# Optimization experiments

Hardware: AMD Instinct MI355X
Metric: run time of the kernel (lower is better)

Reference implementation:

```python
import jax, jax.numpy as jnp
import numpy as np

B = 128        # graphs in batch
GW = 30        # grid width (nodes per graph = GW*GW)
IW = 90        # image width = 3*GW for k=7,s=3,p=2 conv transpose
C_IN = 32
HID = [64, 64, 32]
R = 8          # num relations
NB = 4         # num bases
N = B * GW * GW          # 115200 nodes
E = N * 8                # 921600 edges
NEG_SLOPE = 0.01         # F.leaky_relu default


def setup_inputs() -> dict:
    key = jax.random.key(0)
    ks = jax.random.split(key, 24)
    inp = {
        "features": jax.random.normal(ks[0], (N, C_IN), jnp.float32),
        "src": jax.random.randint(ks[1], (E,), 0, N),
        "dst": jax.random.randint(ks[2], (E,), 0, N),
        "etypes": jax.random.randint(ks[3], (E,), 0, R),
        "norm": jax.random.uniform(ks[4], (E,), jnp.float32),
    }
    dims = [C_IN] + HID
    for l in range(3):
        din, dout = dims[l], dims[l + 1]
        s = 1.0 / np.sqrt(din)
        inp[f"bases{l}"] = jax.random.normal(ks[5 + 4 * l], (NB, din, dout), jnp.float32) * s
        inp[f"comp{l}"] = jax.random.normal(ks[6 + 4 * l], (R, NB), jnp.float32) * (1.0 / np.sqrt(NB))
        inp[f"loop{l}"] = jax.random.normal(ks[7 + 4 * l], (din, dout), jnp.float32) * s
        inp[f"bias{l}"] = jnp.zeros((dout,), jnp.float32)
    inp["conv_w"] = jax.random.normal(ks[20], (HID[-1], 1, 7, 7), jnp.float32) * 0.05  # torch ConvT layout (Cin,Cout,kH,kW)
    inp["conv_b"] = jnp.zeros((1,), jnp.float32)
    return inp


def _rel_graph_conv(h, bases, comp, loop_w, bias, src, dst, etypes, norm, act):
    # basis decomposition: W_r = sum_b comp[r,b] * bases[b]   -> (R, in, out)
    W = jnp.einsum("rb,bio->rio", comp, bases)
    # project every node by every relation weight, then gather per edge
    proj = jnp.einsum("ni,rio->nro", h, W)          # (N, R, out)
    msg = proj[src, etypes] * norm[:, None]          # (E, out)
    agg = jax.ops.segment_sum(msg, dst, num_segments=h.shape[0])
    out = agg + h @ loop_w + bias                    # self-loop + bias (DGL defaults)
    return act(out)


def _conv_transpose(x, w_torch, b, stride, pad):
    # torch ConvTranspose2d(w: (Cin,Cout,kH,kW)) == dilated conv with flipped kernel
    k = w_torch.shape[-1]
    w = jnp.flip(w_torch, (2, 3)).transpose(1, 0, 2, 3)  # -> OIHW
    p = k - 1 - pad
    y = jax.lax.conv_general_dilated(
        x, w, window_strides=(1, 1), padding=[(p, p), (p, p)],
        lhs_dilation=(stride, stride),
        dimension_numbers=("NCHW", "OIHW", "NCHW"))
    return y + b[None, :, None, None]


def reference(features, src, dst, etypes, norm,
              bases0, comp0, loop0, bias0,
              bases1, comp1, loop1, bias1,
              bases2, comp2, loop2, bias2,
              conv_w, conv_b):
    leaky = lambda x: jnp.where(x >= 0, x, NEG_SLOPE * x)
    h = _rel_graph_conv(features, bases0, comp0, loop0, bias0, src, dst, etypes, norm, leaky)
    h = _rel_graph_conv(h, bases1, comp1, loop1, bias1, src, dst, etypes, norm, leaky)
    logits = _rel_graph_conv(h, bases2, comp2, loop2, bias2, src, dst, etypes, norm, jax.nn.sigmoid)
    # every graph has exactly GW*GW nodes -> vectorized decode (replaces per-graph loop)
    x = logits.reshape(B, GW, GW, HID[-1]).transpose(0, 3, 1, 2)  # (B, C, GW, GW)
    y = jax.nn.sigmoid(_conv_transpose(x, conv_w, conv_b, stride=3, pad=2))  # (B,1,IW,IW)
    return y.reshape(B, IW, IW)
```

## Files before the change

### kernel.cpp

```cpp
#include <hip/hip_runtime.h>
#include <hip/hip_bf16.h>

#define B_GR   128
#define GWID   30
#define IWID   90
#define C_IN   32
#define R_REL  8
#define NBAS   4
#define N_NODES (B_GR*GWID*GWID)
#define E_EDGES (N_NODES*8)
#define NEG_SLOPE 0.01f

#define SCAN_BLOCKS (N_NODES/256)

typedef __attribute__((ext_vector_type(8))) __bf16 bf16x8;
typedef __attribute__((ext_vector_type(4))) float f32x4;

__global__ void k_bases_t(const float* __restrict__ bases, __bf16* __restrict__ Bt,
                          int din, int dout) {
    int idx = blockIdx.x*256 + threadIdx.x;
    int tot = NBAS*din*dout;
    if (idx >= tot) return;
    int b = idx/(dout*din), rem = idx%(dout*din);
    int c = rem/din, k = rem%din;
    Bt[idx] = (__bf16)bases[((size_t)b*din + k)*dout + c];
}
__global__ void k_loop_t(const float* __restrict__ loopw, __bf16* __restrict__ loopt,
                         int din, int dout) {
    int idx = blockIdx.x*256 + threadIdx.x;
    if (idx >= din*dout) return;
    int c = idx/din, k = idx%din;
    loopt[idx] = (__bf16)loopw[(size_t)k*dout + c];
}
__global__ void k_feat2bf(const float* __restrict__ f, __bf16* __restrict__ fb) {
    int i = blockIdx.x*256 + threadIdx.x;
    if (i >= N_NODES*C_IN/8) return;
    const float4* p = (const float4*)(f + (size_t)i*8);
    float4 a = p[0], b = p[1];
    bf16x8 o;
    o[0]=(__bf16)a.x; o[1]=(__bf16)a.y; o[2]=(__bf16)a.z; o[3]=(__bf16)a.w;
    o[4]=(__bf16)b.x; o[5]=(__bf16)b.y; o[6]=(__bf16)b.z; o[7]=(__bf16)b.w;
    *(bf16x8*)(fb + (size_t)i*8) = o;
}

__global__ void k_deg(const int* __restrict__ dst, int* __restrict__ deg) {
    int e = blockIdx.x*256 + threadIdx.x;
    if (e < E_EDGES) atomicAdd(&deg[dst[e]], 1);
}
__global__ __launch_bounds__(256) void k_scan1(const int* __restrict__ deg,
                                               int* __restrict__ rowptr,
                                               int* __restrict__ bsum) {
    __shared__ int s[256], s2[256];
    const int tid = threadIdx.x, gid = blockIdx.x*256 + tid;
    int v = deg[gid];
    s[tid] = v;
    __syncthreads();
    int* cur = s; int* nxt = s2;
    for (int d = 1; d < 256; d <<= 1) {
        int val = cur[tid];
        if (tid >= d) val += cur[tid - d];
        nxt[tid] = val;
        __syncthreads();
        int* t = cur; cur = nxt; nxt = t;
    }
    rowptr[gid] = cur[tid] - v;
    if (tid == 255) bsum[blockIdx.x] = cur[255];
}
__global__ __launch_bounds__(512) void k_scan2(int* __restrict__ bsum, int* __restrict__ rowptr) {
    __shared__ int s[512], s2[512];
    const int tid = threadIdx.x;
    int v = (tid < SCAN_BLOCKS) ? bsum[tid] : 0;
    s[tid] = v;
    __syncthreads();
    int* cur = s; int* nxt = s2;
    for (int d = 1; d < 512; d <<= 1) {
        int val = cur[tid];
        if (tid >= d) val += cur[tid - d];
        nxt[tid] = val;
        __syncthreads();
        int* t = cur; cur = nxt; nxt = t;
    }
    if (tid < SCAN_BLOCKS) bsum[tid] = cur[tid] - v;
    if (tid == 0) rowptr[N_NODES] = E_EDGES;
}
__global__ void k_scan3(int* __restrict__ rowptr, const int* __restrict__ bsum,
                        int* __restrict__ cursor) {
    int gid = blockIdx.x*256 + threadIdx.x;
    int v = rowptr[gid] + bsum[blockIdx.x];
    rowptr[gid] = v;
    cursor[gid] = v;
}
__global__ void k_scatter_pack(const int* __restrict__ src, const int* __restrict__ dst,
                               const int* __restrict__ et, const float* __restrict__ norm,
                               int* __restrict__ cursor, int2* __restrict__ pmeta) {
    int e = blockIdx.x*256 + threadIdx.x;
    if (e < E_EDGES) {
        int pos = atomicAdd(&cursor[dst[e]], 1);
        int2 m;
        m.x = src[e] | (et[e] << 24);
        m.y = __float_as_int(norm[e]);
        pmeta[pos] = m;
    }
}

template<int DIN, int DOUT, int ACT, int IN_F32, int OUT_F32, int MINW>
__global__ __launch_bounds__(256, MINW) void k_fusedb(
        const void* __restrict__ hin, const __bf16* __restrict__ Bt,
        const __bf16* __restrict__ loopt, const float* __restrict__ bias,
        const float* __restrict__ comp, const int* __restrict__ rowptr,
        const int2* __restrict__ pmeta, void* __restrict__ hout) {
    constexpr int KS = DIN/32;
    constexpr int NF = DOUT/16;
    const int tid = threadIdx.x;
    const int w = tid >> 6, l = tid & 63;
    const int m = l & 15, g = l >> 4;
    const int nb = blockIdx.x*64 + w*16;
    const int node = nb + m;

    f32x4 acc[NF];
    #pragma unroll
    for (int nf = 0; nf < NF; ++nf) acc[nf] = (f32x4){0.f,0.f,0.f,0.f};

    float ka[NBAS][KS][8];
    #pragma unroll
    for (int b = 0; b < NBAS; ++b)
        #pragma unroll
        for (int ks = 0; ks < KS; ++ks)
            #pragma unroll
            for (int c = 0; c < 8; ++c) ka[b][ks][c] = 0.f;

    const int jb = rowptr[node], je = rowptr[node+1];
    int2 mt = pmeta[jb];
    for (int j = jb; j < je; ++j) {
        const int2 mtn = pmeta[j+1];
        const int p = mt.x & 0xFFFFFF;
        const int et = ((unsigned)mt.x) >> 24;
        const float nm = __int_as_float(mt.y);
        const float4 cw = *(const float4*)(comp + et*NBAS);
        const float w0 = nm*cw.x, w1 = nm*cw.y, w2 = nm*cw.z, w3 = nm*cw.w;
        float hv[KS][8];
        if (IN_F32) {
            const float* hp = (const float*)hin + (size_t)p*DIN + g*8;
            #pragma unroll
            for (int ks = 0; ks < KS; ++ks) {
                float4 v0 = *(const float4*)(hp + ks*32);
                float4 v1 = *(const float4*)(hp + ks*32 + 4);
                hv[ks][0]=v0.x; hv[ks][1]=v0.y; hv[ks][2]=v0.z; hv[ks][3]=v0.w;
                hv[ks][4]=v1.x; hv[ks][5]=v1.y; hv[ks][6]=v1.z; hv[ks][7]=v1.w;
            }
        } else {
            const __bf16* hp = (const __bf16*)hin + (size_t)p*DIN + g*8;
            #pragma unroll
            for (int ks = 0; ks < KS; ++ks) {
                bf16x8 v = *(const bf16x8*)(hp + ks*32);
                #pragma unroll
                for (int c = 0; c < 8; ++c) hv[ks][c] = (float)v[c];
            }
        }
        #pragma unroll
        for (int ks = 0; ks < KS; ++ks) {
            #pragma unroll
            for (int c = 0; c < 8; ++c) {
                ka[0][ks][c] += w0*hv[ks][c];
                ka[1][ks][c] += w1*hv[ks][c];
                ka[2][ks][c] += w2*hv[ks][c];
                ka[3][ks][c] += w3*hv[ks][c];
            }
        }
        mt = mtn;
    }

    #pragma unroll
    for (int b = 0; b < NBAS; ++b) {
        #pragma unroll
        for (int ks = 0; ks < KS; ++ks) {
            bf16x8 fa;
            #pragma unroll
            for (int c = 0; c < 8; ++c) fa[c] = (__bf16)ka[b][ks][c];
            #pragma unroll
            for (int nf = 0; nf < NF; ++nf) {
                bf16x8 fb = *(const bf16x8*)(Bt + ((size_t)b*DOUT + nf*16 + m)*DIN
                                             + ks*32 + g*8);
                acc[nf] = __builtin_amdgcn_mfma_f32_16x16x32_bf16(fa, fb, acc[nf], 0, 0, 0);
            }
        }
    }

    #pragma unroll
    for (int ks = 0; ks < KS; ++ks) {
        bf16x8 fa;
        if (IN_F32) {
            const float* hp = (const float*)hin + (size_t)node*DIN + ks*32 + g*8;
            float4 v0 = *(const float4*)hp;
            float4 v1 = *(const float4*)(hp + 4);
            fa[0]=(__bf16)v0.x; fa[1]=(__bf16)v0.y; fa[2]=(__bf16)v0.z; fa[3]=(__bf16)v0.w;
            fa[4]=(__bf16)v1.x; fa[5]=(__bf16)v1.y; fa[6]=(__bf16)v1.z; fa[7]=(__bf16)v1.w;
        } else {
            fa = *(const bf16x8*)((const __bf16*)hin + (size_t)node*DIN + ks*32 + g*8);
        }
        #pragma unroll
        for (int nf = 0; nf < NF; ++nf) {
            bf16x8 fb = *(const bf16x8*)(loopt + (size_t)(nf*16 + m)*DIN + ks*32 + g*8);
            acc[nf] = __builtin_amdgcn_mfma_f32_16x16x32_bf16(fa, fb, acc[nf], 0, 0, 0);
        }
    }

    #pragma unroll
    for (int nf = 0; nf < NF; ++nf) {
        const int col = nf*16 + m;
        const float bv = bias[col];
        #pragma unroll
        for (int ri = 0; ri < 4; ++ri) {
            const int orow = nb + g*4 + ri;
            float v = acc[nf][ri] + bv;
            if (ACT == 0) v = (v >= 0.f) ? v : NEG_SLOPE*v;
            else          v = 1.f/(1.f + __expf(-v));
            if (OUT_F32) ((float*)hout)[(size_t)orow*DOUT + col] = v;
            else         ((__bf16*)hout)[(size_t)orow*DOUT + col] = (__bf16)v;
        }
    }
}

__global__ __launch_bounds__(256) void k_convt_f32(const float* __restrict__ logits,
        const float* __restrict__ w, const float* __restrict__ cb, float* __restrict__ out) {
    __shared__ float s_w[49*32];
    const int tid = threadIdx.x;
    for (int idx = tid; idx < 49*32; idx += 256) {
        int tap = idx/32, c = idx%32;
        s_w[tap*32 + c] = w[c*49 + tap];
    }
    __syncthreads();
    int gidx = blockIdx.x*256 + tid;
    if (gidx >= B_GR*IWID*IWID) return;
    int b = gidx/(IWID*IWID);
    int rem = gidx%(IWID*IWID);
    int oy = rem/IWID, ox = rem%IWID;

    const int py = (oy+2)%3, qy = (oy+2)/3;
    const int px = (ox+2)%3, qx = (ox+2)/3;

    float acc = cb[0];
    #pragma unroll
    for (int sy = 0; sy < 3; ++sy) {
        const int ky = py + 3*sy;
        const int iy = qy - sy;
        if (ky > 6 || iy < 0 || iy >= GWID) continue;
        #pragma unroll
        for (int sx = 0; sx < 3; ++sx) {
            const int kx = px + 3*sx;
            const int ix = qx - sx;
            if (kx > 6 || ix < 0 || ix >= GWID) continue;
            const float4* xp = (const float4*)&logits[(((size_t)b*GWID + iy)*GWID + ix)*32];
            const float4* wp = (const float4*)&s_w[(ky*7 + kx)*32];
            #pragma unroll
            for (int c4 = 0; c4 < 8; ++c4) {
                float4 xv = xp[c4], wv = wp[c4];
                acc += xv.x*wv.x + xv.y*wv.y + xv.z*wv.z + xv.w*wv.w;
            }
        }
    }
    out[gidx] = 1.f/(1.f + __expf(-acc));
}

extern "C" void kernel_launch(void* const* d_in, const int* in_sizes, int n_in,
                              void* d_out, int out_size, void* d_ws, size_t ws_size,
                              hipStream_t stream) {
    const float* features = (const float*)d_in[0];
    const int*   src      = (const int*)  d_in[1];
    const int*   dst      = (const int*)  d_in[2];
    const int*   etypes   = (const int*)  d_in[3];
    const float* norm     = (const float*)d_in[4];
    const float* bases0 = (const float*)d_in[5];
    const float* comp0  = (const float*)d_in[6];
    const float* loop0  = (const float*)d_in[7];
    const float* bias0  = (const float*)d_in[8];
    const float* bases1 = (const float*)d_in[9];
    const float* comp1  = (const float*)d_in[10];
    const float* loop1  = (const float*)d_in[11];
    const float* bias1  = (const float*)d_in[12];
    const float* bases2 = (const float*)d_in[13];
    const float* comp2  = (const float*)d_in[14];
    const float* loop2  = (const float*)d_in[15];
    const float* bias2  = (const float*)d_in[16];
    const float* conv_w = (const float*)d_in[17];
    const float* conv_b = (const float*)d_in[18];
    float* out = (float*)d_out;

    const int ebl = (E_EDGES + 255)/256;
    float* ws = (float*)d_ws;
    auto pad4 = [](size_t v){ return (v + 3) & ~(size_t)3; };

    size_t off = 0;
    __bf16* Bt0   = (__bf16*)(ws + off); off += (size_t)NBAS*32*64/2;
    __bf16* Bt1   = (__bf16*)(ws + off); off += (size_t)NBAS*64*64/2;
    __bf16* Bt2   = (__bf16*)(ws + off); off += (size_t)NBAS*64*32/2;
    __bf16* lt0   = (__bf16*)(ws + off); off += (size_t)64*32/2;
    __bf16* lt1   = (__bf16*)(ws + off); off += (size_t)64*64/2;
    __bf16* lt2   = (__bf16*)(ws + off); off += (size_t)32*64/2;
    __bf16* fbf   = (__bf16*)(ws + off); off += (size_t)N_NODES*C_IN/2;
    __bf16* h1    = (__bf16*)(ws + off); off += (size_t)N_NODES*64/2;
    __bf16* h2    = (__bf16*)(ws + off); off += (size_t)N_NODES*64/2;
    float*  lg    = (float*)(ws + off);  off += (size_t)N_NODES*32;
    int* rowptr   = (int*)(ws + off); off += pad4((size_t)N_NODES + 4);
    int* deg      = (int*)(ws + off); off += (size_t)N_NODES;
    int* bsum     = (int*)(ws + off); off += 512;
    int2* pmeta   = (int2*)(ws + off); off += (size_t)(E_EDGES + 8)*2;

    k_bases_t<<<(NBAS*32*64 + 255)/256, 256, 0, stream>>>(bases0, Bt0, 32, 64);
    k_bases_t<<<(NBAS*64*64 + 255)/256, 256, 0, stream>>>(bases1, Bt1, 64, 64);
    k_bases_t<<<(NBAS*64*32 + 255)/256, 256, 0, stream>>>(bases2, Bt2, 64, 32);
    k_loop_t<<<(32*64 + 255)/256, 256, 0, stream>>>(loop0, lt0, 32, 64);
    k_loop_t<<<(64*64 + 255)/256, 256, 0, stream>>>(loop1, lt1, 64, 64);
    k_loop_t<<<(64*32 + 255)/256, 256, 0, stream>>>(loop2, lt2, 64, 32);
    k_feat2bf<<<(N_NODES*C_IN/8 + 255)/256, 256, 0, stream>>>(features, fbf);

    hipMemsetAsync(deg, 0, (size_t)N_NODES*sizeof(int), stream);
    k_deg  <<<ebl, 256, 0, stream>>>(dst, deg);
    k_scan1<<<SCAN_BLOCKS, 256, 0, stream>>>(deg, rowptr, bsum);
    k_scan2<<<1, 512, 0, stream>>>(bsum, rowptr);
    k_scan3<<<SCAN_BLOCKS, 256, 0, stream>>>(rowptr, bsum, deg);
    k_scatter_pack<<<ebl, 256, 0, stream>>>(src, dst, etypes, norm, deg, pmeta);

    const int NROWT = N_NODES/64;

    k_fusedb<32,64,0,0,0,4><<<NROWT, 256, 0, stream>>>(fbf, Bt0, lt0, bias0, comp0,
                                                       rowptr, pmeta, h1);
    k_fusedb<64,64,0,0,0,3><<<NROWT, 256, 0, stream>>>(h1, Bt1, lt1, bias1, comp1,
                                                       rowptr, pmeta, h2);
    k_fusedb<64,32,1,0,1,3><<<NROWT, 256, 0, stream>>>(h2, Bt2, lt2, bias2, comp2,
                                                       rowptr, pmeta, lg);

    k_convt_f32<<<(B_GR*IWID*IWID + 255)/256, 256, 0, stream>>>(lg, conv_w, conv_b, out);
}
```

Baseline: 329.5 us.

## Restructure transposed conv by output phase with 3x3 register tiling

The transposed convolution is reorganised so that each block handles one of the nine stride phases, which leaves every thread with a uniform set of kernel taps. Each thread now computes a 3x3 tile of same-phase outputs and reuses a 5x5 window of input vectors and the phase's weights from registers. This cuts the redundant global loads of logits and the per-pixel branching of the old one-output-per-thread kernel. In exchange it raises register pressure, which the added launch-bounds occupancy hint tries to contain, and it gives less parallelism. The grid of 50x256 threads per phase assumes 128x100 tiles exactly.

```diff
diff --git a/kernel.cpp b/kernel.cpp
--- a/kernel.cpp
+++ b/kernel.cpp
@@ -221,7 +221,7 @@
     }
 }
 
-__global__ __launch_bounds__(256) void k_convt_f32(const float* __restrict__ logits,
+__global__ __launch_bounds__(256, 3) void k_convt_ph(const float* __restrict__ logits,
         const float* __restrict__ w, const float* __restrict__ cb, float* __restrict__ out) {
     __shared__ float s_w[49*32];
     const int tid = threadIdx.x;
@@ -230,36 +230,85 @@
         s_w[tap*32 + c] = w[c*49 + tap];
     }
     __syncthreads();
-    int gidx = blockIdx.x*256 + tid;
-    if (gidx >= B_GR*IWID*IWID) return;
-    int b = gidx/(IWID*IWID);
-    int rem = gidx%(IWID*IWID);
-    int oy = rem/IWID, ox = rem%IWID;
-
-    const int py = (oy+2)%3, qy = (oy+2)/3;
-    const int px = (ox+2)%3, qx = (ox+2)/3;
-
-    float acc = cb[0];
-    #pragma unroll
-    for (int sy = 0; sy < 3; ++sy) {
-        const int ky = py + 3*sy;
-        const int iy = qy - sy;
-        if (ky > 6 || iy < 0 || iy >= GWID) continue;
-        #pragma unroll
-        for (int sx = 0; sx < 3; ++sx) {
-            const int kx = px + 3*sx;
-            const int ix = qx - sx;
-            if (kx > 6 || ix < 0 || ix >= GWID) continue;
-            const float4* xp = (const float4*)&logits[(((size_t)b*GWID + iy)*GWID + ix)*32];
-            const float4* wp = (const float4*)&s_w[(ky*7 + kx)*32];
-            #pragma unroll
-            for (int c4 = 0; c4 < 8; ++c4) {
-                float4 xv = xp[c4], wv = wp[c4];
-                acc += xv.x*wv.x + xv.y*wv.y + xv.z*wv.z + xv.w*wv.w;
-            }
-        }
-    }
-    out[gidx] = 1.f/(1.f + __expf(-acc));
+
+    const int phase = blockIdx.y;
+    const int py = phase/3, px = phase%3;
+    const int SY = (py == 0) ? 3 : 2;
+    const int SX = (px == 0) ? 3 : 2;
+    const int qylo = (py == 2) ? 0 : 1;
+    const int qxlo = (px == 2) ? 0 : 1;
+
+    const int idx = blockIdx.x*256 + tid;
+    const int b = idx/100, r = idx%100;
+    const int qy0 = qylo + (r/10)*3;
+    const int qx0 = qxlo + (r%10)*3;
+
+    const float cb0 = cb[0];
+    float acc[3][3];
+    #pragma unroll
+    for (int ry = 0; ry < 3; ++ry)
+        #pragma unroll
+        for (int rx = 0; rx < 3; ++rx) acc[ry][rx] = cb0;
+
+    for (int c4 = 0; c4 < 8; ++c4) {
+        float4 wq[3][3];
+        #pragma unroll
+        for (int sy = 0; sy < 3; ++sy) {
+            if (sy < SY) {
+                #pragma unroll
+                for (int sx = 0; sx < 3; ++sx) {
+                    if (sx < SX)
+                        wq[sy][sx] = *(const float4*)&s_w[((py+3*sy)*7 + px+3*sx)*32 + c4*4];
+                }
+            }
+        }
+        float4 cq[5][5];
+        #pragma unroll
+        for (int dy = 0; dy < 5; ++dy) {
+            if (dy < SY + 2) {
+                const int iy = qy0 + 2 - dy;
+                #pragma unroll
+                for (int dx = 0; dx < 5; ++dx) {
+                    if (dx < SX + 2) {
+                        const int ix = qx0 + 2 - dx;
+                        if (iy >= 0 && iy < GWID && ix >= 0 && ix < GWID)
+                            cq[dy][dx] = *(const float4*)&logits[(((size_t)b*GWID + iy)*GWID + ix)*32 + c4*4];
+                        else
+                            cq[dy][dx] = make_float4(0.f,0.f,0.f,0.f);
+                    }
+                }
+            }
+        }
+        #pragma unroll
+        for (int sy = 0; sy < 3; ++sy) {
+            if (sy < SY) {
+                #pragma unroll
+                for (int sx = 0; sx < 3; ++sx) {
+                    if (sx < SX) {
+                        const float4 wv = wq[sy][sx];
+                        #pragma unroll
+                        for (int ry = 0; ry < 3; ++ry) {
+                            #pragma unroll
+                            for (int rx = 0; rx < 3; ++rx) {
+                                const float4 xv = cq[2-ry+sy][2-rx+sx];
+                                acc[ry][rx] += xv.x*wv.x + xv.y*wv.y + xv.z*wv.z + xv.w*wv.w;
+                            }
+                        }
+                    }
+                }
+            }
+        }
+    }
+
+    #pragma unroll
+    for (int ry = 0; ry < 3; ++ry) {
+        const int oy = 3*(qy0 + ry) + py - 2;
+        #pragma unroll
+        for (int rx = 0; rx < 3; ++rx) {
+            const int ox = 3*(qx0 + rx) + px - 2;
+            out[((size_t)b*IWID + oy)*IWID + ox] = 1.f/(1.f + __expf(-acc[ry][rx]));
+        }
+    }
 }
 
 extern "C" void kernel_launch(void* const* d_in, const int* in_sizes, int n_in,
@@ -330,5 +379,5 @@
     k_fusedb<64,32,1,0,1,3><<<NROWT, 256, 0, stream>>>(h2, Bt2, lt2, bias2, comp2,
                                                        rowptr, pmeta, lg);
 
-    k_convt_f32<<<(B_GR*IWID*IWID + 255)/256, 256, 0, stream>>>(lg, conv_w, conv_b, out);
-}
+    k_convt_ph<<<dim3(50, 9), 256, 0, stream>>>(lg, conv_w, conv_b, out);
+}
```

Result: slower. 512.9 us (+55.7%).
